# Performance work log

Measured on AMD Instinct MI355X. Metric: run time of the kernel, lower is better.

Reference implementation:

```python
import jax, jax.numpy as jnp
import numpy as np

N, E, IN, HID, OUT, H, R = 50000, 800000, 128, 64, 64, 4, 64
NEG_SLOPE = 0.2


def setup_inputs() -> dict:
    key = jax.random.key(0)
    ks = jax.random.split(key, 20)
    s = 0.05
    inp = {
        "x": jax.random.normal(ks[0], (N, IN), jnp.float32),
        "edge_index": jax.random.randint(ks[1], (2, E), 0, N, jnp.int32),
        "edge_type": jax.random.randint(ks[2], (E,), 0, R, jnp.int32),
        # layer 1 (in -> hidden)
        "rel1": jax.random.normal(ks[3], (R, IN), jnp.float32) * s,
        "W1": jax.random.normal(ks[4], (IN, H * HID), jnp.float32) * s,
        "We1": jax.random.normal(ks[5], (IN, H * HID), jnp.float32) * s,
        "as1": jax.random.normal(ks[6], (H, HID), jnp.float32) * s,
        "ad1": jax.random.normal(ks[7], (H, HID), jnp.float32) * s,
        "ae1": jax.random.normal(ks[8], (H, HID), jnp.float32) * s,
        "b1": jnp.zeros((HID,), jnp.float32),
        # layer 2 (hidden -> out)
        "rel2": jax.random.normal(ks[9], (R, HID), jnp.float32) * s,
        "W2": jax.random.normal(ks[10], (HID, H * OUT), jnp.float32) * s,
        "We2": jax.random.normal(ks[11], (HID, H * OUT), jnp.float32) * s,
        "as2": jax.random.normal(ks[12], (H, OUT), jnp.float32) * s,
        "ad2": jax.random.normal(ks[13], (H, OUT), jnp.float32) * s,
        "ae2": jax.random.normal(ks[14], (H, OUT), jnp.float32) * s,
        "b2": jnp.zeros((OUT,), jnp.float32),
    }
    return inp


def gat_layer(x, src, dst, edge_type, rel, W, We, a_s, a_d, a_e, b, C):
    # x: [N, Din] -> per-head features [N, H, C]
    xs = (x @ W).reshape(-1, H, C)
    alpha_src = jnp.einsum('nhc,hc->nh', xs, a_s)   # [N,H]
    alpha_dst = jnp.einsum('nhc,hc->nh', xs, a_d)   # [N,H]
    e = (rel[edge_type] @ We).reshape(-1, H, C)     # [E,H,C] projected edge feats
    alpha_e = jnp.einsum('ehc,hc->eh', e, a_e)      # [E,H]
    logits = alpha_src[src] + alpha_dst[dst] + alpha_e
    logits = jnp.where(logits >= 0, logits, NEG_SLOPE * logits)  # leaky_relu
    # segment softmax over destination nodes
    lmax = jax.ops.segment_max(logits, dst, num_segments=N)      # [N,H]
    ex = jnp.exp(logits - lmax[dst])
    den = jax.ops.segment_sum(ex, dst, num_segments=N)           # [N,H]
    w = ex / den[dst]                                            # [E,H]
    msg = w[:, :, None] * xs[src]                                # [E,H,C]
    out = jax.ops.segment_sum(msg, dst, num_segments=N)          # [N,H,C]
    return out.mean(axis=1) + b                                  # concat=False -> head mean


def reference(x, edge_index, edge_type, rel1, W1, We1, as1, ad1, ae1, b1,
              rel2, W2, We2, as2, ad2, ae2, b2):
    src, dst = edge_index[0], edge_index[1]
    h = gat_layer(x, src, dst, edge_type, rel1, W1, We1, as1, ad1, ae1, b1, HID)
    h = jax.nn.relu(h)
    out = gat_layer(h, src, dst, edge_type, rel2, W2, We2, as2, ad2, ae2, b2, OUT)
    return out
```

## Files before the change

### kernel.cpp

```cpp
#include <hip/hip_runtime.h>
#include <hip/hip_bf16.h>
#include <hip/hip_fp16.h>
#include <math.h>

#define N_NODES 50000
#define N_EDGES 800000
#define IN_DIM 128
#define NHEAD 4
#define NREL 64
#define HC 256
#define NEG_SLOPE 0.2f
#define SCAN_B ((N_NODES + 255) / 256)

__device__ __forceinline__ void load_lds16(const float* g, float* l) {
  __builtin_amdgcn_global_load_lds(
      (const __attribute__((address_space(1))) unsigned int*)g,
      (__attribute__((address_space(3))) unsigned int*)l, 16, 0, 0);
}

__global__ __launch_bounds__(256) void gemm_xw_alpha(
    const float* __restrict__ X, const float* __restrict__ W,
    const float* __restrict__ a_s, const float* __restrict__ a_d,
    __half2* __restrict__ xs16, float* __restrict__ asrc, float* __restrict__ adst,
    int M, int K) {
  __shared__ __align__(16) float wbuf[2][16][128];
  __shared__ __align__(16) float xbuf[2][64][16];
  const int t = threadIdx.x;
  const int wv = t >> 6;
  const int l  = t & 63;
  const int rg = l >> 5;
  const int cg = l & 31;
  const int cc = cg * 4;
  const int rbase = wv * 16 + rg * 8;
  const int row0 = blockIdx.x * 64;
  const int c0 = blockIdx.y * 128;

#define STAGE(BI, KB)                                                          \
  {                                                                            \
    _Pragma("unroll")                                                          \
    for (int j = 0; j < 2; ++j) {                                              \
      const int wrow = wv * 4 + j * 2 + (l >> 5);                              \
      load_lds16(&W[(size_t)((KB) + wrow) * HC + c0 + (l & 31) * 4],           \
                 &wbuf[BI][wv * 4 + j * 2][0]);                                \
    }                                                                          \
    {                                                                          \
      const int xrow = wv * 16 + (l >> 2);                                     \
      const int grow = min(row0 + xrow, M - 1);                                \
      load_lds16(&X[(size_t)grow * K + (KB) + (l & 3) * 4],                    \
                 &xbuf[BI][wv * 16][0]);                                       \
    }                                                                          \
  }

  float acc[8][4];
#pragma unroll
  for (int r = 0; r < 8; ++r)
#pragma unroll
    for (int c = 0; c < 4; ++c) acc[r][c] = 0.f;

  STAGE(0, 0);
  const int nt = K >> 4;
  for (int tg = 0; tg < nt; ++tg) {
    const int cur = tg & 1;
    if (tg + 1 < nt) {
      STAGE(cur ^ 1, (tg + 1) * 16);
      asm volatile("s_waitcnt vmcnt(3)" ::: "memory");
    } else {
      asm volatile("s_waitcnt vmcnt(0)" ::: "memory");
    }
    __builtin_amdgcn_s_barrier();
    __builtin_amdgcn_sched_barrier(0);
#pragma unroll
    for (int kk = 0; kk < 16; ++kk) {
      const float4 w4 = *(const float4*)&wbuf[cur][kk][cc];
      float xr[8];
#pragma unroll
      for (int r = 0; r < 8; ++r) xr[r] = xbuf[cur][rbase + r][kk];
#pragma unroll
      for (int r = 0; r < 8; ++r) {
        acc[r][0] += xr[r] * w4.x;
        acc[r][1] += xr[r] * w4.y;
        acc[r][2] += xr[r] * w4.z;
        acc[r][3] += xr[r] * w4.w;
      }
    }
    asm volatile("" ::: "memory");
    __builtin_amdgcn_s_barrier();
  }
#undef STAGE

  const float4 as4 = *(const float4*)&a_s[c0 + cc];
  const float4 ad4 = *(const float4*)&a_d[c0 + cc];
  const int head = blockIdx.y * 2 + (cg >> 4);
#pragma unroll
  for (int r = 0; r < 8; ++r) {
    const int row = row0 + rbase + r;
    const bool ok = row < M;
    if (ok) {
      __half2 q0 = __floats2half2_rn(acc[r][0], acc[r][1]);
      __half2 q1 = __floats2half2_rn(acc[r][2], acc[r][3]);
      uint2 qq = make_uint2(*(unsigned*)&q0, *(unsigned*)&q1);
      *(uint2*)&xs16[((size_t)row * HC + c0 + cc) >> 1] = qq;
    }
    float sp = acc[r][0] * as4.x + acc[r][1] * as4.y + acc[r][2] * as4.z + acc[r][3] * as4.w;
    float dp = acc[r][0] * ad4.x + acc[r][1] * ad4.y + acc[r][2] * ad4.z + acc[r][3] * ad4.w;
#pragma unroll
    for (int off = 1; off < 16; off <<= 1) {
      sp += __shfl_xor(sp, off);
      dp += __shfl_xor(dp, off);
    }
    if ((cg & 15) == 0 && ok) {
      asrc[row * NHEAD + head] = sp;
      adst[row * NHEAD + head] = dp;
    }
  }
}

__global__ __launch_bounds__(256) void relalpha2_kernel(
    const float* __restrict__ rel1, const float* __restrict__ We1, const float* __restrict__ ae1,
    const float* __restrict__ rel2, const float* __restrict__ We2, const float* __restrict__ ae2,
    float* __restrict__ tab1, float* __restrict__ tab2) {
  const int layer = blockIdx.x >> 6;
  const int r = blockIdx.x & 63;
  const float* rel = layer ? rel2 : rel1;
  const float* We  = layer ? We2  : We1;
  const float* ae  = layer ? ae2  : ae1;
  float* tab       = layer ? tab2 : tab1;
  const int K      = layer ? 64   : IN_DIM;
  int t = threadIdx.x;
  float acc = 0.f;
  for (int k = 0; k < K; ++k) acc += rel[(size_t)r * K + k] * We[(size_t)k * HC + t];
  int h = t >> 6, lane = t & 63;
  float p = acc * ae[t];
#pragma unroll
  for (int off = 32; off > 0; off >>= 1) p += __shfl_down(p, off);
  if (lane == 0) tab[r * NHEAD + h] = p;
}

__global__ __launch_bounds__(256) void hist_kernel(
    const int* __restrict__ dst, int* __restrict__ deg) {
  int e = blockIdx.x * blockDim.x + threadIdx.x;
  if (e < N_EDGES) atomicAdd(&deg[dst[e]], 1);
}

__global__ __launch_bounds__(256) void block_sum_kernel(
    const int* __restrict__ deg, int* __restrict__ bsum) {
  int i = blockIdx.x * 256 + threadIdx.x;
  int v = (i < N_NODES) ? deg[i] : 0;
#pragma unroll
  for (int off = 32; off > 0; off >>= 1) v += __shfl_down(v, off);
  __shared__ int w[4];
  if ((threadIdx.x & 63) == 0) w[threadIdx.x >> 6] = v;
  __syncthreads();
  if (threadIdx.x == 0) bsum[blockIdx.x] = w[0] + w[1] + w[2] + w[3];
}

__global__ __launch_bounds__(256) void scan_bsum_kernel(
    const int* __restrict__ bsum, int* __restrict__ boff) {
  __shared__ int s[256];
  int t = threadIdx.x;
  int v = (t < SCAN_B) ? bsum[t] : 0;
  s[t] = v;
  __syncthreads();
  for (int off = 1; off < 256; off <<= 1) {
    int u = (t >= off) ? s[t - off] : 0;
    __syncthreads();
    s[t] += u;
    __syncthreads();
  }
  boff[t] = (t == 0) ? 0 : s[t - 1];
}

__global__ __launch_bounds__(256) void scan_final_kernel(
    const int* __restrict__ deg, const int* __restrict__ boff,
    int* __restrict__ rowptr, int* __restrict__ cursor) {
  __shared__ int s[256];
  int t = threadIdx.x;
  int i = blockIdx.x * 256 + t;
  int v = (i < N_NODES) ? deg[i] : 0;
  s[t] = v;
  __syncthreads();
  for (int off = 1; off < 256; off <<= 1) {
    int u = (t >= off) ? s[t - off] : 0;
    __syncthreads();
    s[t] += u;
    __syncthreads();
  }
  int excl = boff[blockIdx.x] + s[t] - v;
  if (i < N_NODES) {
    rowptr[i] = excl;
    cursor[i] = excl;
  }
  if (t == 0 && blockIdx.x == 0) rowptr[N_NODES] = N_EDGES;
}

__global__ __launch_bounds__(256) void fill_kernel(
    const int* __restrict__ src, const int* __restrict__ dst,
    const int* __restrict__ etype, int* __restrict__ cursor,
    int2* __restrict__ csr_pack) {
  int e = blockIdx.x * blockDim.x + threadIdx.x;
  if (e >= N_EDGES) return;
  int d = dst[e];
  int i = atomicAdd(&cursor[d], 1);
  csr_pack[i] = make_int2(src[e], etype[e]);
}

__global__ __launch_bounds__(256) void gat_node_kernel(
    const int* __restrict__ rowptr, const int2* __restrict__ csr,
    const float* __restrict__ asrc, const float* __restrict__ adst,
    const float* __restrict__ tab, const __half2* __restrict__ xs16,
    const float* __restrict__ b, float* __restrict__ out, int relu) {
  const int n = (blockIdx.x * blockDim.x + threadIdx.x) >> 6;
  if (n >= N_NODES) return;
  const int lane = threadIdx.x & 63;
  const int hh = lane >> 4;
  const int cbase = lane << 2;
  const int i0 = rowptr[n], i1 = rowptr[n + 1];
  const float adn = adst[n * NHEAD + hh];
  const float treg = tab[lane * NHEAD + hh];

  float4 acc = make_float4(0.f, 0.f, 0.f, 0.f);
  float den = 0.f;
  int i = i0;
  for (; i + 4 <= i1; i += 4) {
    const int2 p0 = csr[i], p1 = csr[i + 1], p2 = csr[i + 2], p3 = csr[i + 3];
    float l0 = asrc[p0.x * NHEAD + hh] + adn + __shfl(treg, p0.y);
    float l1 = asrc[p1.x * NHEAD + hh] + adn + __shfl(treg, p1.y);
    float l2 = asrc[p2.x * NHEAD + hh] + adn + __shfl(treg, p2.y);
    float l3 = asrc[p3.x * NHEAD + hh] + adn + __shfl(treg, p3.y);
    const uint2 q0 = *(const uint2*)&xs16[((size_t)p0.x * HC + cbase) >> 1];
    const uint2 q1 = *(const uint2*)&xs16[((size_t)p1.x * HC + cbase) >> 1];
    const uint2 q2 = *(const uint2*)&xs16[((size_t)p2.x * HC + cbase) >> 1];
    const uint2 q3 = *(const uint2*)&xs16[((size_t)p3.x * HC + cbase) >> 1];
    l0 = (l0 >= 0.f) ? l0 : NEG_SLOPE * l0;
    l1 = (l1 >= 0.f) ? l1 : NEG_SLOPE * l1;
    l2 = (l2 >= 0.f) ? l2 : NEG_SLOPE * l2;
    l3 = (l3 >= 0.f) ? l3 : NEG_SLOPE * l3;
    const float w0 = __expf(l0), w1 = __expf(l1), w2 = __expf(l2), w3 = __expf(l3);
    den += (w0 + w1) + (w2 + w3);
    const float2 a0 = __half22float2(*(const __half2*)&q0.x), b0 = __half22float2(*(const __half2*)&q0.y);
    const float2 a1 = __half22float2(*(const __half2*)&q1.x), b1 = __half22float2(*(const __half2*)&q1.y);
    const float2 a2 = __half22float2(*(const __half2*)&q2.x), b2 = __half22float2(*(const __half2*)&q2.y);
    const float2 a3 = __half22float2(*(const __half2*)&q3.x), b3 = __half22float2(*(const __half2*)&q3.y);
    acc.x += w0 * a0.x + w1 * a1.x + w2 * a2.x + w3 * a3.x;
    acc.y += w0 * a0.y + w1 * a1.y + w2 * a2.y + w3 * a3.y;
    acc.z += w0 * b0.x + w1 * b1.x + w2 * b2.x + w3 * b3.x;
    acc.w += w0 * b0.y + w1 * b1.y + w2 * b2.y + w3 * b3.y;
  }
  for (; i < i1; ++i) {
    const int2 p = csr[i];
    float l = asrc[p.x * NHEAD + hh] + adn + __shfl(treg, p.y);
    l = (l >= 0.f) ? l : NEG_SLOPE * l;
    const float w = __expf(l);
    const uint2 q = *(const uint2*)&xs16[((size_t)p.x * HC + cbase) >> 1];
    const float2 a = __half22float2(*(const __half2*)&q.x);
    const float2 c = __half22float2(*(const __half2*)&q.y);
    den += w;
    acc.x += w * a.x; acc.y += w * a.y; acc.z += w * c.x; acc.w += w * c.y;
  }

  const float rd = (den > 0.f) ? (0.25f / den) : 0.f;
  float4 y = make_float4(acc.x * rd, acc.y * rd, acc.z * rd, acc.w * rd);
#pragma unroll
  for (int off = 16; off < 64; off <<= 1) {
    y.x += __shfl_xor(y.x, off);
    y.y += __shfl_xor(y.y, off);
    y.z += __shfl_xor(y.z, off);
    y.w += __shfl_xor(y.w, off);
  }
  if (lane < 16) {
    const float4 bb = *(const float4*)&b[lane * 4];
    y.x += bb.x; y.y += bb.y; y.z += bb.z; y.w += bb.w;
    if (relu) {
      y.x = fmaxf(y.x, 0.f); y.y = fmaxf(y.y, 0.f);
      y.z = fmaxf(y.z, 0.f); y.w = fmaxf(y.w, 0.f);
    }
    *(float4*)&out[(size_t)n * 64 + lane * 4] = y;
  }
}

extern "C" void kernel_launch(void* const* d_in, const int* in_sizes, int n_in,
                              void* d_out, int out_size, void* d_ws, size_t ws_size,
                              hipStream_t stream) {
  const float* x   = (const float*)d_in[0];
  const int* eidx  = (const int*)d_in[1];
  const int* etype = (const int*)d_in[2];
  const float* rel1 = (const float*)d_in[3];
  const float* W1   = (const float*)d_in[4];
  const float* We1  = (const float*)d_in[5];
  const float* as1  = (const float*)d_in[6];
  const float* ad1  = (const float*)d_in[7];
  const float* ae1  = (const float*)d_in[8];
  const float* b1   = (const float*)d_in[9];
  const float* rel2 = (const float*)d_in[10];
  const float* W2   = (const float*)d_in[11];
  const float* We2  = (const float*)d_in[12];
  const float* as2  = (const float*)d_in[13];
  const float* ad2  = (const float*)d_in[14];
  const float* ae2  = (const float*)d_in[15];
  const float* b2   = (const float*)d_in[16];
  const int* src = eidx;
  const int* dst = eidx + N_EDGES;

  __half2* xs16 = (__half2*)d_ws;
  float* fbase = (float*)((char*)d_ws + (size_t)N_NODES * HC * 2);
  float* asrc = fbase;
  float* adst = asrc + (size_t)N_NODES * NHEAD;
  float* tab1 = adst + (size_t)N_NODES * NHEAD;
  float* tab2 = tab1 + NREL * NHEAD;
  float* h1   = tab2 + NREL * NHEAD;
  int* ip = (int*)(h1 + (size_t)N_NODES * 64);
  int* deg     = ip;
  int* rowptr  = deg + N_NODES;
  int* cursor  = rowptr + N_NODES + 1;
  int2* csr    = (int2*)(cursor + N_NODES + 1);
  int* bsum    = (int*)(csr + N_EDGES);
  int* boff    = bsum + 256;

  hipMemsetAsync(deg, 0, N_NODES * sizeof(int), stream);
  hist_kernel<<<(N_EDGES + 255) / 256, 256, 0, stream>>>(dst, deg);
  block_sum_kernel<<<SCAN_B, 256, 0, stream>>>(deg, bsum);
  scan_bsum_kernel<<<1, 256, 0, stream>>>(bsum, boff);
  scan_final_kernel<<<SCAN_B, 256, 0, stream>>>(deg, boff, rowptr, cursor);
  fill_kernel<<<(N_EDGES + 255) / 256, 256, 0, stream>>>(src, dst, etype, cursor, csr);
  relalpha2_kernel<<<2 * NREL, 256, 0, stream>>>(rel1, We1, ae1, rel2, We2, ae2, tab1, tab2);

  const dim3 gemm_grid((N_NODES + 63) / 64, 2);
  const int GB = (N_NODES * 64 + 255) / 256;

  gemm_xw_alpha<<<gemm_grid, 256, 0, stream>>>(x, W1, as1, ad1, xs16, asrc, adst, N_NODES, IN_DIM);
  gat_node_kernel<<<GB, 256, 0, stream>>>(rowptr, csr, asrc, adst, tab1, xs16, b1, h1, 1);

  gemm_xw_alpha<<<gemm_grid, 256, 0, stream>>>(h1, W2, as2, ad2, xs16, asrc, adst, N_NODES, 64);
  gat_node_kernel<<<GB, 256, 0, stream>>>(rowptr, csr, asrc, adst, tab2, xs16, b2, (float*)d_out, 0);
}
```

Measured before the change: 339.6 us.

## Retile GEMM to full-width columns, read X rows directly instead of via LDS

The node-projection GEMM now has each block cover all 256 output columns for 32 rows, rather than 64 rows by 128 columns over a 2-wide y grid. Only W is staged through LDS. Each wave reads its 8 X rows straight from global memory as wave-uniform broadcast loads. This removes the duplicated X reads across the column-split blocks and the X LDS staging traffic. In exchange, the X loads are no longer prefetched asynchronously and may stall the FMA loop, and W is reloaded by twice as many blocks.

```diff
diff --git a/kernel.cpp b/kernel.cpp
--- a/kernel.cpp
+++ b/kernel.cpp
@@ -23,32 +23,29 @@
     const float* __restrict__ a_s, const float* __restrict__ a_d,
     __half2* __restrict__ xs16, float* __restrict__ asrc, float* __restrict__ adst,
     int M, int K) {
-  __shared__ __align__(16) float wbuf[2][16][128];
-  __shared__ __align__(16) float xbuf[2][64][16];
+  __shared__ __align__(16) float wbuf[2][16][256];
   const int t = threadIdx.x;
-  const int wv = t >> 6;
-  const int l  = t & 63;
-  const int rg = l >> 5;
-  const int cg = l & 31;
-  const int cc = cg * 4;
-  const int rbase = wv * 16 + rg * 8;
-  const int row0 = blockIdx.x * 64;
-  const int c0 = blockIdx.y * 128;
-
-#define STAGE(BI, KB)                                                          \
-  {                                                                            \
-    _Pragma("unroll")                                                          \
-    for (int j = 0; j < 2; ++j) {                                              \
-      const int wrow = wv * 4 + j * 2 + (l >> 5);                              \
-      load_lds16(&W[(size_t)((KB) + wrow) * HC + c0 + (l & 31) * 4],           \
-                 &wbuf[BI][wv * 4 + j * 2][0]);                                \
-    }                                                                          \
-    {                                                                          \
-      const int xrow = wv * 16 + (l >> 2);                                     \
-      const int grow = min(row0 + xrow, M - 1);                                \
-      load_lds16(&X[(size_t)grow * K + (KB) + (l & 3) * 4],                    \
-                 &xbuf[BI][wv * 16][0]);                                       \
-    }                                                                          \
+  const int wv = __builtin_amdgcn_readfirstlane(t >> 6);
+  const int lane = t & 63;
+  const int cc = lane * 4;
+  const int row0 = blockIdx.x * 32;
+  const int rbase = row0 + wv * 8;
+
+  const float* Xr[8];
+#pragma unroll
+  for (int r = 0; r < 8; ++r) {
+    int grow = rbase + r;
+    grow = (grow < M) ? grow : (M - 1);
+    Xr[r] = X + (size_t)grow * K;
+  }
+
+#define STAGE(BI, KB)                                                         \
+  {                                                                           \
+    _Pragma("unroll")                                                         \
+    for (int j = 0; j < 4; ++j) {                                             \
+      const int kk = wv * 4 + j;                                              \
+      load_lds16(&W[(size_t)((KB) + kk) * HC + lane * 4], &wbuf[BI][kk][0]);  \
+    }                                                                         \
   }
 
   float acc[8][4];
@@ -61,26 +58,32 @@
   const int nt = K >> 4;
   for (int tg = 0; tg < nt; ++tg) {
     const int cur = tg & 1;
+    const int kb = tg * 16;
     if (tg + 1 < nt) {
-      STAGE(cur ^ 1, (tg + 1) * 16);
-      asm volatile("s_waitcnt vmcnt(3)" ::: "memory");
+      STAGE(cur ^ 1, kb + 16);
+      asm volatile("s_waitcnt vmcnt(4)" ::: "memory");
     } else {
       asm volatile("s_waitcnt vmcnt(0)" ::: "memory");
     }
     __builtin_amdgcn_s_barrier();
     __builtin_amdgcn_sched_barrier(0);
 #pragma unroll
-    for (int kk = 0; kk < 16; ++kk) {
-      const float4 w4 = *(const float4*)&wbuf[cur][kk][cc];
-      float xr[8];
-#pragma unroll
-      for (int r = 0; r < 8; ++r) xr[r] = xbuf[cur][rbase + r][kk];
-#pragma unroll
-      for (int r = 0; r < 8; ++r) {
-        acc[r][0] += xr[r] * w4.x;
-        acc[r][1] += xr[r] * w4.y;
-        acc[r][2] += xr[r] * w4.z;
-        acc[r][3] += xr[r] * w4.w;
+    for (int q = 0; q < 4; ++q) {
+      float xr[8][4];
+#pragma unroll
+      for (int r = 0; r < 8; ++r)
+#pragma unroll
+        for (int j = 0; j < 4; ++j) xr[r][j] = Xr[r][kb + q * 4 + j];
+#pragma unroll
+      for (int j = 0; j < 4; ++j) {
+        const float4 w4 = *(const float4*)&wbuf[cur][q * 4 + j][cc];
+#pragma unroll
+        for (int r = 0; r < 8; ++r) {
+          acc[r][0] += xr[r][j] * w4.x;
+          acc[r][1] += xr[r][j] * w4.y;
+          acc[r][2] += xr[r][j] * w4.z;
+          acc[r][3] += xr[r][j] * w4.w;
+        }
       }
     }
     asm volatile("" ::: "memory");
@@ -88,18 +91,18 @@
   }
 #undef STAGE
 
-  const float4 as4 = *(const float4*)&a_s[c0 + cc];
-  const float4 ad4 = *(const float4*)&a_d[c0 + cc];
-  const int head = blockIdx.y * 2 + (cg >> 4);
+  const float4 as4 = *(const float4*)&a_s[cc];
+  const float4 ad4 = *(const float4*)&a_d[cc];
+  const int head = lane >> 4;
 #pragma unroll
   for (int r = 0; r < 8; ++r) {
-    const int row = row0 + rbase + r;
+    const int row = rbase + r;
     const bool ok = row < M;
     if (ok) {
       __half2 q0 = __floats2half2_rn(acc[r][0], acc[r][1]);
       __half2 q1 = __floats2half2_rn(acc[r][2], acc[r][3]);
       uint2 qq = make_uint2(*(unsigned*)&q0, *(unsigned*)&q1);
-      *(uint2*)&xs16[((size_t)row * HC + c0 + cc) >> 1] = qq;
+      *(uint2*)&xs16[((size_t)row * HC + cc) >> 1] = qq;
     }
     float sp = acc[r][0] * as4.x + acc[r][1] * as4.y + acc[r][2] * as4.z + acc[r][3] * as4.w;
     float dp = acc[r][0] * ad4.x + acc[r][1] * ad4.y + acc[r][2] * ad4.z + acc[r][3] * ad4.w;
@@ -108,7 +111,7 @@
       sp += __shfl_xor(sp, off);
       dp += __shfl_xor(dp, off);
     }
-    if ((cg & 15) == 0 && ok) {
+    if ((lane & 15) == 0 && ok) {
       asrc[row * NHEAD + head] = sp;
       adst[row * NHEAD + head] = dp;
     }
@@ -324,7 +327,7 @@
   fill_kernel<<<(N_EDGES + 255) / 256, 256, 0, stream>>>(src, dst, etype, cursor, csr);
   relalpha2_kernel<<<2 * NREL, 256, 0, stream>>>(rel1, We1, ae1, rel2, We2, ae2, tab1, tab2);
 
-  const dim3 gemm_grid((N_NODES + 63) / 64, 2);
+  const dim3 gemm_grid((N_NODES + 31) / 32);
   const int GB = (N_NODES * 64 + 255) / 256;
 
   gemm_xw_alpha<<<gemm_grid, 256, 0, stream>>>(x, W1, as1, ad1, xs16, asrc, adst, N_NODES, IN_DIM);
```

Result: slower. 424.9 us (+25.1%).
